# Performance work log

Measured on AMD Instinct MI355X. Metric: run time of the kernel, lower is better.

The kernel has to match this reference:

```python
import jax, jax.numpy as jnp
import numpy as np

B, Hh, Ww, C = 16, 56, 56, 384
HEADS, WS, SHIFT = 12, 7, 3
N = WS * WS            # 49 tokens per window
NW = (Hh // WS) * (Ww // WS)  # 64 windows
HID = int(C * 4.0)
SCALE = (C // HEADS) ** -0.5
EPS = 1e-5


def _relative_position_index():
    coords = np.stack(np.meshgrid(np.arange(WS), np.arange(WS), indexing='ij')).reshape(2, -1)
    rel = (coords[:, :, None] - coords[:, None, :]).transpose(1, 2, 0)  # (N,N,2)
    rel[..., 0] += WS - 1
    rel[..., 1] += WS - 1
    rel[..., 0] *= 2 * WS - 1
    return jnp.asarray(rel.sum(-1))  # (N,N) int

RPI = _relative_position_index()


def _swin_mask():
    img = np.zeros((Hh, Ww), np.float32)
    slices = (slice(0, -WS), slice(-WS, -SHIFT), slice(-SHIFT, None))
    cnt = 0
    for hs in slices:
        for ws in slices:
            img[hs, ws] = cnt
            cnt += 1
    m = img.reshape(Hh // WS, WS, Ww // WS, WS).transpose(0, 2, 1, 3).reshape(-1, N)  # (nW,N)
    am = m[:, None, :] - m[:, :, None]
    return jnp.asarray(np.where(am != 0, -100.0, 0.0).astype(np.float32))  # (nW,N,N)


def setup_inputs() -> dict:
    key = jax.random.key(0)
    ks = jax.random.split(key, 12)
    p = lambda k, shp, s=0.02: (jax.random.normal(k, shp, jnp.float32) * s)
    return {
        'x': jax.random.normal(ks[0], (B, Hh * Ww, C), jnp.float32),
        'mask_matrix': _swin_mask(),
        'norm1_g': jnp.ones((C,), jnp.float32),
        'norm1_b': jnp.zeros((C,), jnp.float32),
        'qkv_w': p(ks[1], (3 * C, C)),
        'qkv_b': jnp.zeros((3 * C,), jnp.float32),
        'rpb_table': p(ks[2], ((2 * WS - 1) * (2 * WS - 1), HEADS)),
        'proj_w': p(ks[3], (C, C)),
        'proj_b': jnp.zeros((C,), jnp.float32),
        'norm2_g': jnp.ones((C,), jnp.float32),
        'norm2_b': jnp.zeros((C,), jnp.float32),
        'fc1_w': p(ks[4], (HID, C)),
        'fc1_b': jnp.zeros((HID,), jnp.float32),
        'fc2_w': p(ks[5], (C, HID)),
        'fc2_b': jnp.zeros((C,), jnp.float32),
    }


def _ln(x, g, b):
    m = jnp.mean(x, -1, keepdims=True)
    v = jnp.mean(jnp.square(x - m), -1, keepdims=True)
    return (x - m) * jax.lax.rsqrt(v + EPS) * g + b


def reference(x, mask_matrix, norm1_g, norm1_b, qkv_w, qkv_b, rpb_table,
              proj_w, proj_b, norm2_g, norm2_b, fc1_w, fc1_b, fc2_w, fc2_b):
    shortcut = x
    h = _ln(x, norm1_g, norm1_b).reshape(B, Hh, Ww, C)
    # cyclic shift (H,W divisible by window -> no pad)
    h = jnp.roll(h, (-SHIFT, -SHIFT), axis=(1, 2))
    # window partition -> (B*nW, N, C)
    win = h.reshape(B, Hh // WS, WS, Ww // WS, WS, C).transpose(0, 1, 3, 2, 4, 5).reshape(-1, N, C)
    B_ = win.shape[0]
    hd = C // HEADS
    qkv = (win @ qkv_w.T + qkv_b).reshape(B_, N, 3, HEADS, hd).transpose(2, 0, 3, 1, 4)
    q, k, v = qkv[0] * SCALE, qkv[1], qkv[2]  # (B_,H,N,hd)
    attn = jnp.einsum('bhnd,bhmd->bhnm', q, k)  # (B_,H,N,N)
    bias = rpb_table[RPI]  # (N,N,heads)
    attn = attn + bias.transpose(2, 0, 1)[None]
    attn = attn.reshape(B, NW, HEADS, N, N) + mask_matrix[None, :, None]
    attn = jax.nn.softmax(attn.reshape(B_, HEADS, N, N), axis=-1)
    out = jnp.einsum('bhnm,bhmd->bhnd', attn, v).transpose(0, 2, 1, 3).reshape(B_, N, C)
    out = out @ proj_w.T + proj_b
    # window reverse + reverse shift
    out = out.reshape(B, Hh // WS, Ww // WS, WS, WS, C).transpose(0, 1, 3, 2, 4, 5).reshape(B, Hh, Ww, C)
    out = jnp.roll(out, (SHIFT, SHIFT), axis=(1, 2)).reshape(B, Hh * Ww, C)
    x = shortcut + out
    h2 = _ln(x, norm2_g, norm2_b)
    h2 = jax.nn.gelu(h2 @ fc1_w.T + fc1_b, approximate=False)  # torch nn.GELU exact
    return x + (h2 @ fc2_w.T + fc2_b)
```

## Files before the change

### kernel.cpp

```cpp
#include <hip/hip_runtime.h>

typedef unsigned short u16;
typedef unsigned int u32;
typedef short s16x8 __attribute__((ext_vector_type(8)));
typedef float f32x4 __attribute__((ext_vector_type(4)));

#define ATTN_SCALE 0.17677669529663687f

__device__ __forceinline__ u16 f2bf(float f) {
  union { float f; u32 i; } c; c.f = f;
  u32 r = c.i + 0x7fffu + ((c.i >> 16) & 1u);
  return (u16)(r >> 16);
}
__device__ __forceinline__ float bf2f(u16 u) {
  union { u32 i; float f; } c; c.i = ((u32)u) << 16; return c.f;
}
__device__ __forceinline__ f32x4 mfma16(s16x8 a, s16x8 b, f32x4 c) {
  return __builtin_amdgcn_mfma_f32_16x16x32_bf16(a, b, c, 0, 0, 0);
}

typedef __attribute__((address_space(1))) u32 gas_u32;
typedef __attribute__((address_space(3))) u32 las_u32;
#define GLL16(gp, lp) __builtin_amdgcn_global_load_lds((gas_u32*)(gp), (las_u32*)(lp), 16, 0, 0)

__device__ __forceinline__ int win_to_orig(int m) {
  int b = m / 3136, rem = m - b * 3136;
  int w = rem / 49, n = rem - w * 49;
  int wh = w >> 3, ww = w & 7;
  int i = n / 7, j = n - i * 7;
  int r = wh * 7 + i + 3; if (r >= 56) r -= 56;
  int c = ww * 7 + j + 3; if (c >= 56) c -= 56;
  return b * 3136 + r * 56 + c;
}

__global__ __launch_bounds__(256) void cvt_all_kernel(
    const float* __restrict__ qkvw, const float* __restrict__ projw,
    const float* __restrict__ fc1w, const float* __restrict__ fc2w,
    u16* __restrict__ wq, u16* __restrict__ wp,
    u16* __restrict__ w1, u16* __restrict__ w2) {
  int i = blockIdx.x * 256 + threadIdx.x;
  if (i < 442368) wq[i] = f2bf(qkvw[i]);
  else if (i < 589824) wp[i - 442368] = f2bf(projw[i - 442368]);
  else if (i < 1179648) w1[i - 589824] = f2bf(fc1w[i - 589824]);
  else if (i < 1769472) w2[i - 1179648] = f2bf(fc2w[i - 1179648]);
}

template <bool PERM, bool BFIN>
__global__ __launch_bounds__(256) void ln_kernel(
    const void* __restrict__ xin, const float* __restrict__ g,
    const float* __restrict__ bb, u16* __restrict__ xo) {
  int t = blockIdx.x * 4 + (threadIdx.x >> 6);
  int l = threadIdx.x & 63;
  int src = PERM ? win_to_orig(t) : t;
  float v[6];
  if (BFIN) {
    const u16* row = (const u16*)xin + (size_t)src * 384;
#pragma unroll
    for (int k = 0; k < 6; k++) v[k] = bf2f(row[l + 64 * k]);
  } else {
    const float* row = (const float*)xin + (size_t)src * 384;
#pragma unroll
    for (int k = 0; k < 6; k++) v[k] = row[l + 64 * k];
  }
  float s = 0.f;
#pragma unroll
  for (int k = 0; k < 6; k++) s += v[k];
#pragma unroll
  for (int d = 1; d < 64; d <<= 1) s += __shfl_xor(s, d);
  float mean = s * (1.f / 384.f);
  float q = 0.f;
#pragma unroll
  for (int k = 0; k < 6; k++) { float dv = v[k] - mean; q += dv * dv; }
#pragma unroll
  for (int d = 1; d < 64; d <<= 1) q += __shfl_xor(q, d);
  float rstd = rsqrtf(q * (1.f / 384.f) + 1e-5f);
  u16* orow = xo + (size_t)t * 384;
#pragma unroll
  for (int k = 0; k < 6; k++) {
    int c = l + 64 * k;
    orow[c] = f2bf((v[k] - mean) * rstd * g[c] + bb[c]);
  }
}

template <int EPI>
__global__ __launch_bounds__(256) void gemm_kernel(
    const u16* __restrict__ A, const u16* __restrict__ W,
    const float* __restrict__ bias, u16* __restrict__ outb,
    float* __restrict__ outf, const float* __restrict__ auxf,
    const u16* __restrict__ auxb, int K, int N, int NT, int NB) {
  __shared__ __align__(16) short As[8192];
  __shared__ __align__(16) short Bs[8192];
  const int tid = threadIdx.x, wv = tid >> 6, l = tid & 63;
  const int lr = l & 15, lg = l >> 4;
  int bm, bn;
  {
    const int STS = NT << 3;
    const int body = (NB >> 3) * STS;
    int d = blockIdx.x;
    if (d < body) {
      int st = d / STS, rem = d - st * STS;
      bn = rem >> 3;
      bm = st * 8 + (rem & 7);
    } else {
      int t = d - body;
      int tq = t / NT;
      bm = (NB & ~7) + tq;
      bn = t - tq * NT;
    }
  }
  const size_t m0 = (size_t)bm * 128, n0 = (size_t)bn * 128;
  const int prow = wv * 16 + (l >> 2);
  const int ccl = (((l & 3) ^ ((l >> 3) & 3)) << 3);
  const u16* ga0 = A + (m0 + prow) * K + ccl;
  const u16* ga1 = A + (m0 + 64 + prow) * K + ccl;
  const u16* gb0 = W + (n0 + prow) * K + ccl;
  const u16* gb1 = W + (n0 + 64 + prow) * K + ccl;
  const int stoff = wv * 512;
  const int wr = wv >> 1, wc = wv & 1;
  const int sw = (lr >> 1) & 3;
  const int aoff = (wr * 64 + lr) * 32 + ((lg ^ sw) << 3);
  const int boff = (wc * 64 + lr) * 32 + ((lg ^ sw) << 3);

#define STAGE(bufo, koff)                            \
  do {                                               \
    GLL16(ga0 + (koff), As + (bufo) + stoff);        \
    GLL16(ga1 + (koff), As + (bufo) + 2048 + stoff); \
    GLL16(gb0 + (koff), Bs + (bufo) + stoff);        \
    GLL16(gb1 + (koff), Bs + (bufo) + 2048 + stoff); \
  } while (0)
#define FRAG_READS(cur)                                              \
  do {                                                               \
    const short* as = As + (cur);                                    \
    const short* bs = Bs + (cur);                                    \
    _Pragma("unroll") for (int mi = 0; mi < 4; mi++)                 \
        af[mi] = *(const s16x8*)&as[aoff + mi * (16 * 32)];          \
    _Pragma("unroll") for (int ni = 0; ni < 4; ni++)                 \
        bfr[ni] = *(const s16x8*)&bs[boff + ni * (16 * 32)];         \
  } while (0)
#define MFMA_TILE()                                        \
  do {                                                     \
    _Pragma("unroll") for (int mi = 0; mi < 4; mi++)       \
        _Pragma("unroll") for (int ni = 0; ni < 4; ni++)   \
            acc[mi][ni] = mfma16(af[mi], bfr[ni], acc[mi][ni]); \
  } while (0)

  f32x4 acc[4][4] = {};
  s16x8 af[4], bfr[4];
  STAGE(0, 0);
  STAGE(4096, 32);
  int cur = 0;
  int k0 = 0;
  for (; k0 < K - 32; k0 += 32) {
    asm volatile("s_waitcnt vmcnt(4)" ::: "memory");
    __builtin_amdgcn_sched_barrier(0);
    __builtin_amdgcn_s_barrier();
    FRAG_READS(cur);
    asm volatile("s_waitcnt lgkmcnt(0)" ::: "memory");
    __builtin_amdgcn_sched_barrier(0);
    __builtin_amdgcn_s_barrier();
    if (k0 + 64 < K) STAGE(cur, k0 + 64);
    MFMA_TILE();
    cur ^= 4096;
  }
  asm volatile("s_waitcnt vmcnt(0)" ::: "memory");
  __builtin_amdgcn_sched_barrier(0);
  __builtin_amdgcn_s_barrier();
  FRAG_READS(cur);
  asm volatile("s_waitcnt lgkmcnt(0)" ::: "memory");
  __builtin_amdgcn_sched_barrier(0);
  MFMA_TILE();
#undef STAGE
#undef FRAG_READS
#undef MFMA_TILE

  const int colb = (int)n0 + wc * 64;
#pragma unroll
  for (int mi = 0; mi < 4; mi++) {
#pragma unroll
    for (int r = 0; r < 4; r++) {
      const size_t m = m0 + wr * 64 + mi * 16 + lg * 4 + r;
      int dst = 0;
      if (EPI == 1) dst = win_to_orig((int)m);
#pragma unroll
      for (int ni = 0; ni < 4; ni++) {
        const int col = colb + ni * 16 + lr;
        float v = acc[mi][ni][r] + bias[col];
        if (EPI == 0) {
          outb[m * (size_t)N + col] = f2bf(v);
        } else if (EPI == 1) {
          outb[(size_t)dst * 384 + col] = f2bf(v + auxf[(size_t)dst * 384 + col]);
        } else if (EPI == 2) {
          float u = v * (0.7978845608028654f + 0.0356774081f * v * v);
          float gl = v / (1.f + __expf(-2.f * u));
          outb[m * (size_t)N + col] = f2bf(gl);
        } else {
          outf[m * (size_t)N + col] = v + bf2f(auxb[m * (size_t)N + col]);
        }
      }
    }
  }
}

__global__ __launch_bounds__(256) void attn_kernel(
    const u16* __restrict__ qkv, const float* __restrict__ rpb,
    const float* __restrict__ maskp, u16* __restrict__ out) {
  __shared__ __align__(16) short Pl[4][16 * 76];
  __shared__ float rpbs[169 * 12];
  const int tid = threadIdx.x, wv = tid >> 6, l = tid & 63;
  const int lr = l & 15, lg = l >> 4;
  for (int idx = tid; idx < 169 * 12; idx += 256) rpbs[idx] = rpb[idx];
  __syncthreads();

  const int task = blockIdx.x * 4 + wv;
  const int win = task / 12, h = task - win * 12;
  const int wi = win & 63;
  const short* base = (const short*)qkv + (size_t)win * 49 * 1152 + h * 32;

  s16x8 qf[4], kf[4];
  const s16x8 zz = {0, 0, 0, 0, 0, 0, 0, 0};
#pragma unroll
  for (int mi = 0; mi < 4; mi++) {
    int n = mi * 16 + lr;
    if (n < 49) {
      qf[mi] = *(const s16x8*)(base + (size_t)n * 1152 + lg * 8);
      kf[mi] = *(const s16x8*)(base + (size_t)n * 1152 + 384 + lg * 8);
    } else { qf[mi] = zz; kf[mi] = zz; }
  }

  f32x4 acc[4][4] = {};
#pragma unroll
  for (int mi = 0; mi < 4; mi++)
#pragma unroll
    for (int ni = 0; ni < 4; ni++)
      acc[mi][ni] = mfma16(qf[mi], kf[ni], acc[mi][ni]);

  s16x8 vb[2][2];
#pragma unroll
  for (int kk = 0; kk < 2; kk++)
#pragma unroll
    for (int nd = 0; nd < 2; nd++)
#pragma unroll
      for (int e = 0; e < 8; e++) {
        int j = kk * 32 + lg * 8 + e;
        vb[kk][nd][e] = (j < 49)
            ? base[(size_t)j * 1152 + 768 + nd * 16 + lr] : (short)0;
      }

  short* pl = Pl[wv];
#pragma unroll
  for (int mi = 0; mi < 4; mi++) {
    float rs[4];
#pragma unroll
    for (int r = 0; r < 4; r++) {
      const int irow = mi * 16 + lg * 4 + r;
      float sv[4];
      if (irow < 49) {
        const int yi = irow / 7, xi = irow - yi * 7;
        const float* mrow = maskp + ((size_t)wi * 49 + irow) * 49;
#pragma unroll
        for (int ni = 0; ni < 4; ni++) {
          const int j = ni * 16 + lr;
          if (j < 49) {
            int yj = j / 7, xj = j - yj * 7;
            int rpi = (yi - yj + 6) * 13 + (xi - xj + 6);
            sv[ni] = acc[mi][ni][r] * ATTN_SCALE + rpbs[rpi * 12 + h] + mrow[j];
          } else sv[ni] = -1e30f;
        }
      } else {
#pragma unroll
        for (int ni = 0; ni < 4; ni++) sv[ni] = -1e30f;
      }
      float mx = fmaxf(fmaxf(sv[0], sv[1]), fmaxf(sv[2], sv[3]));
#pragma unroll
      for (int d = 1; d < 16; d <<= 1) mx = fmaxf(mx, __shfl_xor(mx, d));
      float sm = 0.f;
#pragma unroll
      for (int ni = 0; ni < 4; ni++) { sv[ni] = __expf(sv[ni] - mx); sm += sv[ni]; }
#pragma unroll
      for (int d = 1; d < 16; d <<= 1) sm += __shfl_xor(sm, d);
      rs[r] = 1.f / sm;
#pragma unroll
      for (int ni = 0; ni < 4; ni++)
        pl[(lg * 4 + r) * 76 + ni * 16 + lr] = (short)f2bf(sv[ni]);
    }
    f32x4 o[2] = {{}, {}};
#pragma unroll
    for (int kk = 0; kk < 2; kk++) {
      s16x8 pa = *(const s16x8*)&pl[lr * 76 + kk * 32 + lg * 8];
#pragma unroll
      for (int nd = 0; nd < 2; nd++)
        o[nd] = mfma16(pa, vb[kk][nd], o[nd]);
    }
#pragma unroll
    for (int r = 0; r < 4; r++) {
      const int irow = mi * 16 + lg * 4 + r;
      if (irow < 49) {
#pragma unroll
        for (int nd = 0; nd < 2; nd++)
          out[((size_t)win * 49 + irow) * 384 + h * 32 + nd * 16 + lr] =
              f2bf(o[nd][r] * rs[r]);
      }
    }
  }
}

extern "C" void kernel_launch(void* const* d_in, const int* in_sizes, int n_in,
                              void* d_out, int out_size, void* d_ws, size_t ws_size,
                              hipStream_t stream) {
  (void)in_sizes; (void)n_in; (void)out_size; (void)ws_size;
  const float* x     = (const float*)d_in[0];
  const float* maskp = (const float*)d_in[1];
  const float* n1g   = (const float*)d_in[2];
  const float* n1b   = (const float*)d_in[3];
  const float* qkvw  = (const float*)d_in[4];
  const float* qkvb  = (const float*)d_in[5];
  const float* rpb   = (const float*)d_in[6];
  const float* projw = (const float*)d_in[7];
  const float* projb = (const float*)d_in[8];
  const float* n2g   = (const float*)d_in[9];
  const float* n2b   = (const float*)d_in[10];
  const float* fc1w  = (const float*)d_in[11];
  const float* fc1b  = (const float*)d_in[12];
  const float* fc2w  = (const float*)d_in[13];
  const float* fc2b  = (const float*)d_in[14];
  float* outp = (float*)d_out;

  char* ws = (char*)d_ws;
  u16*  regA  = (u16*)ws;
  u16*  regB  = (u16*)(ws + 115605504ull);
  u16*  xresb = (u16*)(ws + 154140672ull);
  u16*  wq = (u16*)(ws + 192675840ull);
  u16*  wp = wq + 442368;
  u16*  w1 = wp + 147456;
  u16*  w2 = w1 + 589824;

  cvt_all_kernel<<<6912, 256, 0, stream>>>(qkvw, projw, fc1w, fc2w, wq, wp, w1, w2);
  ln_kernel<true, false><<<12544, 256, 0, stream>>>(x, n1g, n1b, regB);
  gemm_kernel<0><<<392 * 9, 256, 0, stream>>>(regB, wq, qkvb, regA, nullptr,
                                              nullptr, nullptr, 384, 1152, 9, 392);
  attn_kernel<<<3072, 256, 0, stream>>>(regA, rpb, maskp, regB);
  gemm_kernel<1><<<392 * 3, 256, 0, stream>>>(regB, wp, projb, xresb, nullptr,
                                              x, nullptr, 384, 384, 3, 392);
  ln_kernel<false, true><<<12544, 256, 0, stream>>>(xresb, n2g, n2b, regB);
  for (int c = 0; c < 2; c++) {
    const u16* aln = regB + (size_t)c * 25088 * 384;
    float* oc = outp + (size_t)c * 25088 * 384;
    const u16* rc = xresb + (size_t)c * 25088 * 384;
    gemm_kernel<2><<<196 * 12, 256, 0, stream>>>(aln, w1, fc1b, regA, nullptr,
                                                 nullptr, nullptr, 384, 1536, 12, 196);
    gemm_kernel<3><<<196 * 3, 256, 0, stream>>>(regA, w2, fc2b, nullptr, oc,
                                                nullptr, rc, 1536, 384, 3, 196);
  }
}
```

Before: 437.8 us.

## Precompute combined bf16 bias+mask table and prefetch it in attention

Adds a kernel that builds a per-(window,head) bf16 table holding relative-position bias plus shift mask, laid out to match the MFMA fragment order. The attention kernel then does one vector load per row instead of index arithmetic, shared-memory rpb lookups and fp32 mask reads. It also drops the shared-memory rpb staging and its barrier, hoists and unconditionalizes the V loads, prefetches table rows one step ahead, and raises wave priority around the MFMA sections. The cost is an extra launch writing about 6 MB of table each call. Bias and mask are also rounded to bf16, and the V loads now read padded rows past 49 without a guard.

```diff
diff --git a/kernel.cpp b/kernel.cpp
--- a/kernel.cpp
+++ b/kernel.cpp
@@ -3,6 +3,7 @@
 typedef unsigned short u16;
 typedef unsigned int u32;
 typedef short s16x8 __attribute__((ext_vector_type(8)));
+typedef unsigned short u16x4 __attribute__((ext_vector_type(4)));
 typedef float f32x4 __attribute__((ext_vector_type(4)));
 
 #define ATTN_SCALE 0.17677669529663687f
@@ -43,6 +44,26 @@
   else if (i < 589824) wp[i - 442368] = f2bf(projw[i - 442368]);
   else if (i < 1179648) w1[i - 589824] = f2bf(fc1w[i - 589824]);
   else if (i < 1769472) w2[i - 1179648] = f2bf(fc2w[i - 1179648]);
+}
+
+__global__ __launch_bounds__(256) void mk_tbl_kernel(
+    const float* __restrict__ rpb, const float* __restrict__ maskp,
+    u16* __restrict__ tbl) {
+  int idx = blockIdx.x * 256 + threadIdx.x;
+  int wh = idx >> 12;
+  int rem = idx & 4095;
+  int irow = rem >> 6;
+  int lr = (rem >> 2) & 15, ni = rem & 3;
+  int j = ni * 16 + lr;
+  int wi = wh / 12, h = wh - wi * 12;
+  float val = -1e30f;
+  if (irow < 49 && j < 49) {
+    int yi = irow / 7, xi = irow - yi * 7;
+    int yj = j / 7, xj = j - yj * 7;
+    int rpi = (yi - yj + 6) * 13 + (xi - xj + 6);
+    val = rpb[rpi * 12 + h] + maskp[((size_t)wi * 49 + irow) * 49 + j];
+  }
+  tbl[idx] = f2bf(val);
 }
 
 template <bool PERM, bool BFIN>
@@ -202,19 +223,17 @@
 }
 
 __global__ __launch_bounds__(256) void attn_kernel(
-    const u16* __restrict__ qkv, const float* __restrict__ rpb,
-    const float* __restrict__ maskp, u16* __restrict__ out) {
+    const u16* __restrict__ qkv, const u16* __restrict__ tbl,
+    u16* __restrict__ out) {
   __shared__ __align__(16) short Pl[4][16 * 76];
-  __shared__ float rpbs[169 * 12];
   const int tid = threadIdx.x, wv = tid >> 6, l = tid & 63;
   const int lr = l & 15, lg = l >> 4;
-  for (int idx = tid; idx < 169 * 12; idx += 256) rpbs[idx] = rpb[idx];
-  __syncthreads();
 
   const int task = blockIdx.x * 4 + wv;
   const int win = task / 12, h = task - win * 12;
   const int wi = win & 63;
   const short* base = (const short*)qkv + (size_t)win * 49 * 1152 + h * 32;
+  const u16* tb = tbl + (size_t)(wi * 12 + h) * 4096 + lr * 4;
 
   s16x8 qf[4], kf[4];
   const s16x8 zz = {0, 0, 0, 0, 0, 0, 0, 0};
@@ -226,50 +245,43 @@
       kf[mi] = *(const s16x8*)(base + (size_t)n * 1152 + 384 + lg * 8);
     } else { qf[mi] = zz; kf[mi] = zz; }
   }
+  s16x8 vb[2][2];
+#pragma unroll
+  for (int kk = 0; kk < 2; kk++)
+#pragma unroll
+    for (int nd = 0; nd < 2; nd++)
+#pragma unroll
+      for (int e = 0; e < 8; e++)
+        vb[kk][nd][e] = base[(size_t)(kk * 32 + lg * 8 + e) * 1152 + 768 + nd * 16 + lr];
+  u16x4 t4[4][4];
+#pragma unroll
+  for (int r = 0; r < 4; r++)
+    t4[0][r] = *(const u16x4*)&tb[(lg * 4 + r) * 64];
 
   f32x4 acc[4][4] = {};
+  __builtin_amdgcn_s_setprio(1);
 #pragma unroll
   for (int mi = 0; mi < 4; mi++)
 #pragma unroll
     for (int ni = 0; ni < 4; ni++)
       acc[mi][ni] = mfma16(qf[mi], kf[ni], acc[mi][ni]);
-
-  s16x8 vb[2][2];
-#pragma unroll
-  for (int kk = 0; kk < 2; kk++)
-#pragma unroll
-    for (int nd = 0; nd < 2; nd++)
-#pragma unroll
-      for (int e = 0; e < 8; e++) {
-        int j = kk * 32 + lg * 8 + e;
-        vb[kk][nd][e] = (j < 49)
-            ? base[(size_t)j * 1152 + 768 + nd * 16 + lr] : (short)0;
-      }
+  __builtin_amdgcn_s_setprio(0);
 
   short* pl = Pl[wv];
 #pragma unroll
   for (int mi = 0; mi < 4; mi++) {
+    if (mi < 3) {
+#pragma unroll
+      for (int r = 0; r < 4; r++)
+        t4[mi + 1][r] = *(const u16x4*)&tb[((mi + 1) * 16 + lg * 4 + r) * 64];
+    }
     float rs[4];
 #pragma unroll
     for (int r = 0; r < 4; r++) {
-      const int irow = mi * 16 + lg * 4 + r;
       float sv[4];
-      if (irow < 49) {
-        const int yi = irow / 7, xi = irow - yi * 7;
-        const float* mrow = maskp + ((size_t)wi * 49 + irow) * 49;
-#pragma unroll
-        for (int ni = 0; ni < 4; ni++) {
-          const int j = ni * 16 + lr;
-          if (j < 49) {
-            int yj = j / 7, xj = j - yj * 7;
-            int rpi = (yi - yj + 6) * 13 + (xi - xj + 6);
-            sv[ni] = acc[mi][ni][r] * ATTN_SCALE + rpbs[rpi * 12 + h] + mrow[j];
-          } else sv[ni] = -1e30f;
-        }
-      } else {
-#pragma unroll
-        for (int ni = 0; ni < 4; ni++) sv[ni] = -1e30f;
-      }
+#pragma unroll
+      for (int ni = 0; ni < 4; ni++)
+        sv[ni] = acc[mi][ni][r] * ATTN_SCALE + bf2f(t4[mi][r][ni]);
       float mx = fmaxf(fmaxf(sv[0], sv[1]), fmaxf(sv[2], sv[3]));
 #pragma unroll
       for (int d = 1; d < 16; d <<= 1) mx = fmaxf(mx, __shfl_xor(mx, d));
@@ -284,6 +296,7 @@
         pl[(lg * 4 + r) * 76 + ni * 16 + lr] = (short)f2bf(sv[ni]);
     }
     f32x4 o[2] = {{}, {}};
+    __builtin_amdgcn_s_setprio(1);
 #pragma unroll
     for (int kk = 0; kk < 2; kk++) {
       s16x8 pa = *(const s16x8*)&pl[lr * 76 + kk * 32 + lg * 8];
@@ -291,6 +304,7 @@
       for (int nd = 0; nd < 2; nd++)
         o[nd] = mfma16(pa, vb[kk][nd], o[nd]);
     }
+    __builtin_amdgcn_s_setprio(0);
 #pragma unroll
     for (int r = 0; r < 4; r++) {
       const int irow = mi * 16 + lg * 4 + r;
@@ -333,12 +347,14 @@
   u16*  wp = wq + 442368;
   u16*  w1 = wp + 147456;
   u16*  w2 = w1 + 589824;
+  u16*  tbl = w2 + 589824;
 
   cvt_all_kernel<<<6912, 256, 0, stream>>>(qkvw, projw, fc1w, fc2w, wq, wp, w1, w2);
+  mk_tbl_kernel<<<12288, 256, 0, stream>>>(rpb, maskp, tbl);
   ln_kernel<true, false><<<12544, 256, 0, stream>>>(x, n1g, n1b, regB);
   gemm_kernel<0><<<392 * 9, 256, 0, stream>>>(regB, wq, qkvb, regA, nullptr,
                                               nullptr, nullptr, 384, 1152, 9, 392);
-  attn_kernel<<<3072, 256, 0, stream>>>(regA, rpb, maskp, regB);
+  attn_kernel<<<3072, 256, 0, stream>>>(regA, tbl, regB);
   gemm_kernel<1><<<392 * 3, 256, 0, stream>>>(regB, wp, projb, xresb, nullptr,
                                               x, nullptr, 384, 384, 3, 392);
   ln_kernel<false, true><<<12544, 256, 0, stream>>>(xresb, n2g, n2b, regB);
```

Measured after the change: 409.4 us. 1.07x faster.
